# Kernel optimization log

Hardware: AMD Instinct MI355X
Metric: run time of the kernel (lower is better)

Reference implementation:

```python
import jax, jax.numpy as jnp
import numpy as np

B, S, D = 4, 2048, 1024
H, HD = 16, 64
MLP = 4 * D
EPS = 1e-6


def _rms_norm(x, scale):
    var = jnp.mean(jnp.square(x), axis=-1, keepdims=True)
    return x * jax.lax.rsqrt(var + EPS) * scale


def setup_inputs() -> dict:
    key = jax.random.key(0)
    ks = jax.random.split(key, 8)
    sd = D ** -0.5
    return {
        "x": jax.random.normal(ks[0], (B, S, D), jnp.float32),
        "pre_norm_scale": jnp.ones((D,), jnp.float32),
        "w_mlp_in": jax.random.normal(ks[1], (D, MLP), jnp.float32) * sd,   # MLPBlockInput, no bias
        "wq": jax.random.normal(ks[2], (D, H, HD), jnp.float32) * sd,
        "wk": jax.random.normal(ks[3], (D, H, HD), jnp.float32) * sd,
        "wv": jax.random.normal(ks[4], (D, H, HD), jnp.float32) * sd,
        "w_mlp_out": jax.random.normal(ks[5], (MLP, D), jnp.float32) * (MLP ** -0.5),
        "b_mlp_out": jnp.zeros((D,), jnp.float32),
        "w_attn_out": jax.random.normal(ks[6], (H, HD, D), jnp.float32) * sd,  # DenseGeneral axis=(-2,-1)
        "b_attn_out": jnp.zeros((D,), jnp.float32),
    }


def reference(x, pre_norm_scale, w_mlp_in, wq, wk, wv, w_mlp_out, b_mlp_out,
              w_attn_out, b_attn_out):
    residual = x
    xn = _rms_norm(x, pre_norm_scale)                      # pre_norm (TPNorm)

    # QKVMLPDense: fused MLP-input + QKV projections
    h = jax.nn.gelu(jnp.einsum("bsd,df->bsf", xn, w_mlp_in))   # [B,S,MLP]
    q = jnp.einsum("bsd,dhk->bshk", xn, wq)                    # [B,S,H,HD]
    k = jnp.einsum("bsd,dhk->bshk", xn, wk)
    v = jnp.einsum("bsd,dhk->bshk", xn, wv)

    # dot_product_attention (mask=None)
    scores = jnp.einsum("bqhd,bkhd->bhqk", q, k) / jnp.sqrt(jnp.asarray(HD, x.dtype))
    probs = jax.nn.softmax(scores, axis=-1)
    attn_v = jnp.einsum("bhqk,bkhd->bqhd", probs, v)           # [B,S,H,HD]

    # AttnMLPOut: mlp_out + attn_out
    mlp_out = jnp.einsum("bsf,fd->bsd", h, w_mlp_out) + b_mlp_out
    attn_out = jnp.einsum("bqhk,hkd->bqd", attn_v, w_attn_out) + b_attn_out
    block_out = mlp_out + attn_out                              # dropout is identity (train=False)
    return residual + block_out
```

## Files before the change

### kernel.cpp

```cpp
#include <hip/hip_runtime.h>
#include <cstdint>
#include <cstddef>

typedef float floatx4 __attribute__((ext_vector_type(4)));
typedef short bf16x8 __attribute__((ext_vector_type(8)));

#define MFMA(a, b, c) __builtin_amdgcn_mfma_f32_16x16x32_bf16((a), (b), (c), 0, 0, 0)

__device__ __forceinline__ unsigned short f2bf(float f) {
  union { float f; unsigned int u; } v; v.f = f;
  unsigned int u = v.u;
  unsigned int r = (u + 0x7FFFu + ((u >> 16) & 1u)) >> 16;
  return (unsigned short)r;
}

__device__ __forceinline__ void gload_lds16(const unsigned short* g, unsigned short* s) {
  __builtin_amdgcn_global_load_lds(
      (const __attribute__((address_space(1))) unsigned int*)g,
      (__attribute__((address_space(3))) unsigned int*)s, 16, 0, 0);
}

__global__ __launch_bounds__(256) void transpose_cast(
    const float* __restrict__ src, unsigned short* __restrict__ dst,
    int R, int C, int ldd) {
  __shared__ float tile[32][33];
  int bx = blockIdx.x, by = blockIdx.y;
  int tx = threadIdx.x & 31, ty = threadIdx.x >> 5;
#pragma unroll
  for (int i = 0; i < 4; i++) {
    int r = ty + i * 8;
    tile[r][tx] = src[(size_t)(by * 32 + r) * C + bx * 32 + tx];
  }
  __syncthreads();
#pragma unroll
  for (int i = 0; i < 4; i++) {
    int r = ty + i * 8;
    dst[(size_t)(bx * 32 + r) * ldd + by * 32 + tx] = f2bf(tile[tx][r]);
  }
}

__global__ __launch_bounds__(256) void rmsnorm_kernel(
    const float* __restrict__ x, const float* __restrict__ scale,
    unsigned short* __restrict__ xn) {
  int row = blockIdx.x;
  const float4 v = ((const float4*)(x + (size_t)row * 1024))[threadIdx.x];
  float ss = v.x * v.x + v.y * v.y + v.z * v.z + v.w * v.w;
#pragma unroll
  for (int off = 1; off < 64; off <<= 1) ss += __shfl_xor(ss, off, 64);
  __shared__ float ws4[4];
  if ((threadIdx.x & 63) == 0) ws4[threadIdx.x >> 6] = ss;
  __syncthreads();
  float tot = ws4[0] + ws4[1] + ws4[2] + ws4[3];
  float rs = rsqrtf(tot * (1.0f / 1024.0f) + 1e-6f);
  const float4 sc = ((const float4*)scale)[threadIdx.x];
  uint2 o;
  o.x = (unsigned)f2bf(v.x * rs * sc.x) | ((unsigned)f2bf(v.y * rs * sc.y) << 16);
  o.y = (unsigned)f2bf(v.z * rs * sc.z) | ((unsigned)f2bf(v.w * rs * sc.w) << 16);
  ((uint2*)(xn + (size_t)row * 1024))[threadIdx.x] = o;
}

template <int MODE>
__global__ __launch_bounds__(256, 2) void gemm_bt(
    const unsigned short* __restrict__ A, const unsigned short* __restrict__ BT,
    int K, void* __restrict__ outp,
    const float* __restrict__ bias1, const float* __restrict__ bias2,
    const float* __restrict__ resid,
    int msplit, int tm, int tn,
    unsigned short* __restrict__ q_out, unsigned short* __restrict__ k_out,
    unsigned short* __restrict__ v_out) {
  __shared__ unsigned short As[2][128 * 32];
  __shared__ unsigned short Bs[2][128 * 32];

  int id = blockIdx.x + gridDim.x * blockIdx.y;
  int xcd = id & 7, j = id >> 3;
  int mh = xcd % msplit, nq = xcd / msplit;
  int by = mh * tm + j / tn;
  int bx = nq * tn + j % tn;
  int m0 = by * 128, n0 = bx * 128;

  int t = threadIdx.x, lane = t & 63, wave = t >> 6;
  int l15 = lane & 15, quad = lane >> 4;
  int wm = (wave & 1) * 64, wn = (wave >> 1) * 64;

  floatx4 acc[4][4] = {};

  int off0 = wave * 1024 + lane * 8;
  int off1 = off0 + 512;
  int r0 = off0 >> 5, c0 = off0 & 31;
  const unsigned short* gA0 = A + (size_t)(m0 + r0) * K + c0;
  const unsigned short* gA1 = A + (size_t)(m0 + r0 + 16) * K + c0;
  const unsigned short* gB0 = BT + (size_t)(n0 + r0) * K + c0;
  const unsigned short* gB1 = BT + (size_t)(n0 + r0 + 16) * K + c0;
  unsigned short* sA[2] = {&As[0][off0], &As[1][off0]};
  unsigned short* sA_[2] = {&As[0][off1], &As[1][off1]};
  unsigned short* sB[2] = {&Bs[0][off0], &Bs[1][off0]};
  unsigned short* sB_[2] = {&Bs[0][off1], &Bs[1][off1]};

  for (int kt = 0; kt < K; kt += 64) {
    __syncthreads();
#pragma unroll
    for (int kk = 0; kk < 2; kk++) {
      int kg = kt + kk * 32;
      gload_lds16(gA0 + kg, sA[kk]);
      gload_lds16(gA1 + kg, sA_[kk]);
      gload_lds16(gB0 + kg, sB[kk]);
      gload_lds16(gB1 + kg, sB_[kk]);
    }
    __syncthreads();
#pragma unroll
    for (int kk = 0; kk < 2; kk++) {
      bf16x8 a[4], b[4];
#pragma unroll
      for (int im = 0; im < 4; im++)
        a[im] = *(const bf16x8*)&As[kk][(wm + im * 16 + l15) * 32 + quad * 8];
#pragma unroll
      for (int in_ = 0; in_ < 4; in_++)
        b[in_] = *(const bf16x8*)&Bs[kk][(wn + in_ * 16 + l15) * 32 + quad * 8];
#pragma unroll
      for (int im = 0; im < 4; im++)
#pragma unroll
        for (int in_ = 0; in_ < 4; in_++)
          acc[im][in_] = MFMA(a[im], b[in_], acc[im][in_]);
    }
  }

#pragma unroll
  for (int im = 0; im < 4; im++) {
#pragma unroll
    for (int in_ = 0; in_ < 4; in_++) {
#pragma unroll
      for (int r = 0; r < 4; r++) {
        int row = m0 + wm + im * 16 + quad * 4 + r;
        int col = n0 + wn + in_ * 16 + l15;
        float v = acc[im][in_][r];
        if constexpr (MODE == 6) {
          if (n0 < 4096) {
            float z = 0.7978845608028654f * (v + 0.044715f * v * v * v);
            float e = __expf(2.0f * z);
            float th = 1.0f - 2.0f / (e + 1.0f);
            ((unsigned short*)outp)[(size_t)row * 5120 + col] = f2bf(0.5f * v * (1.0f + th));
          } else {
            int seg = (n0 - 4096) >> 10;
            int cs = col - 4096 - (seg << 10);
            int b_ = row >> 11, s = row & 2047, h = cs >> 6, hd = cs & 63;
            if (seg == 0)
              q_out[(((size_t)(b_ * 16 + h)) * 2048 + s) * 64 + hd] = f2bf(v * 0.125f);
            else if (seg == 1)
              k_out[(((size_t)(b_ * 16 + h)) * 2048 + s) * 64 + hd] = f2bf(v);
            else
              v_out[(((size_t)(b_ * 16 + h)) * 64 + hd) * 2048 + s] = f2bf(v);
          }
        } else {
          size_t idx = (size_t)row * 1024 + col;
          ((float*)outp)[idx] = v + bias1[col] + bias2[col] + resid[idx];
        }
      }
    }
  }
}

__global__ __launch_bounds__(256, 2) void flash_attn(
    const unsigned short* __restrict__ q_buf, const unsigned short* __restrict__ k_buf,
    const unsigned short* __restrict__ v_buf, unsigned short* __restrict__ cat) {
  constexpr int S = 2048, HD = 64;
  constexpr int LK = 72, LV = 72, LP = 68;
  __shared__ unsigned short Ks[64 * LK];
  __shared__ unsigned short Vs[64 * LV];
  __shared__ unsigned short Ps[4][32 * LP];

  int id = blockIdx.x + gridDim.x * blockIdx.y;
  int xcd = id & 7, j = id >> 3;
  int bh = xcd * 8 + (j >> 4);
  int qbk = j & 15;

  int t = threadIdx.x, lane = t & 63, wave = t >> 6;
  int l15 = lane & 15, quad = lane >> 4;

  const unsigned short* qp = q_buf + (size_t)bh * S * HD;
  const unsigned short* kp = k_buf + (size_t)bh * S * HD;
  const unsigned short* vp = v_buf + (size_t)bh * HD * S;

  int q0 = qbk * 128 + wave * 32;
  bf16x8 aQ[2][2];
#pragma unroll
  for (int qf = 0; qf < 2; qf++) {
    aQ[qf][0] = *(const bf16x8*)&qp[(size_t)(q0 + qf * 16 + l15) * HD + quad * 8];
    aQ[qf][1] = *(const bf16x8*)&qp[(size_t)(q0 + qf * 16 + l15) * HD + 32 + quad * 8];
  }

  floatx4 acc_o[2][4] = {};
  float lrow[2][4] = {};

  int kr = t >> 3, kc = (t & 7) * 8;

  for (int kv = 0; kv < S; kv += 64) {
    __syncthreads();
#pragma unroll
    for (int i = 0; i < 2; i++) {
      int r = kr + 32 * i;
      *(uint4*)&Ks[r * LK + kc] = *(const uint4*)&kp[(size_t)(kv + r) * HD + kc];
      *(uint4*)&Vs[r * LV + kc] = *(const uint4*)&vp[(size_t)r * S + kv + kc];
    }
    __syncthreads();

    floatx4 z[2][4];
#pragma unroll
    for (int cg = 0; cg < 4; cg++) {
      bf16x8 bk0 = *(const bf16x8*)&Ks[(cg * 16 + l15) * LK + quad * 8];
      bf16x8 bk1 = *(const bf16x8*)&Ks[(cg * 16 + l15) * LK + 32 + quad * 8];
#pragma unroll
      for (int qf = 0; qf < 2; qf++) {
        floatx4 acc = {};
        acc = MFMA(aQ[qf][0], bk0, acc);
        acc = MFMA(aQ[qf][1], bk1, acc);
        z[qf][cg] = acc;
      }
    }
#pragma unroll
    for (int qf = 0; qf < 2; qf++)
#pragma unroll
      for (int cg = 0; cg < 4; cg++)
#pragma unroll
        for (int r = 0; r < 4; r++) {
          float e = __expf(z[qf][cg][r]);
          lrow[qf][r] += e;
          Ps[wave][(qf * 16 + quad * 4 + r) * LP + cg * 16 + l15] = f2bf(e);
        }
    __syncthreads();
#pragma unroll
    for (int c = 0; c < 2; c++) {
      bf16x8 aP[2];
#pragma unroll
      for (int qf = 0; qf < 2; qf++) {
        const unsigned short* pp = &Ps[wave][(qf * 16 + l15) * LP + c * 32 + quad * 8];
        ((uint2*)&aP[qf])[0] = *(const uint2*)pp;
        ((uint2*)&aP[qf])[1] = *(const uint2*)(pp + 4);
      }
#pragma unroll
      for (int n = 0; n < 4; n++) {
        bf16x8 bv = *(const bf16x8*)&Vs[(n * 16 + l15) * LV + c * 32 + quad * 8];
        acc_o[0][n] = MFMA(aP[0], bv, acc_o[0][n]);
        acc_o[1][n] = MFMA(aP[1], bv, acc_o[1][n]);
      }
    }
  }

#pragma unroll
  for (int qf = 0; qf < 2; qf++)
#pragma unroll
    for (int r = 0; r < 4; r++) {
      float s = lrow[qf][r];
#pragma unroll
      for (int off = 1; off < 16; off <<= 1) s += __shfl_xor(s, off, 16);
      lrow[qf][r] = s;
    }

  int b_ = bh >> 4, h = bh & 15;
#pragma unroll
  for (int qf = 0; qf < 2; qf++)
#pragma unroll
    for (int r = 0; r < 4; r++) {
      float inv = 1.0f / lrow[qf][r];
      int srow = q0 + qf * 16 + quad * 4 + r;
      size_t base = ((size_t)(b_ * 2048 + srow)) * 5120 + 4096 + h * 64;
#pragma unroll
      for (int n = 0; n < 4; n++)
        cat[base + n * 16 + l15] = f2bf(acc_o[qf][n][r] * inv);
    }
}

extern "C" void kernel_launch(void* const* d_in, const int* in_sizes, int n_in,
                              void* d_out, int out_size, void* d_ws, size_t ws_size,
                              hipStream_t stream) {
  (void)in_sizes; (void)n_in; (void)out_size; (void)ws_size;
  const float* x          = (const float*)d_in[0];
  const float* pns        = (const float*)d_in[1];
  const float* w_mlp_in   = (const float*)d_in[2];
  const float* wq         = (const float*)d_in[3];
  const float* wk         = (const float*)d_in[4];
  const float* wv         = (const float*)d_in[5];
  const float* w_mlp_out  = (const float*)d_in[6];
  const float* b_mlp_out  = (const float*)d_in[7];
  const float* w_attn_out = (const float*)d_in[8];
  const float* b_attn_out = (const float*)d_in[9];
  float* out = (float*)d_out;

  char* ws = (char*)d_ws;
  size_t off = 0;
  auto alloc = [&](size_t bytes) {
    void* p = ws + off;
    off += (bytes + 255) & ~(size_t)255;
    return p;
  };
  const size_t M = 8192;
  unsigned short* xn     = (unsigned short*)alloc(M * 1024 * 2);
  unsigned short* wcatT  = (unsigned short*)alloc((size_t)7168 * 1024 * 2);
  unsigned short* wcat2T = (unsigned short*)alloc((size_t)1024 * 5120 * 2);
  unsigned short* cat    = (unsigned short*)alloc(M * 5120 * 2);
  unsigned short* qb     = (unsigned short*)alloc(M * 1024 * 2);
  unsigned short* kb     = (unsigned short*)alloc(M * 1024 * 2);
  unsigned short* vb     = (unsigned short*)alloc(M * 1024 * 2);

  transpose_cast<<<dim3(128, 32), 256, 0, stream>>>(w_mlp_in, wcatT, 1024, 4096, 1024);
  transpose_cast<<<dim3(32, 32), 256, 0, stream>>>(wq, wcatT + (size_t)4096 * 1024, 1024, 1024, 1024);
  transpose_cast<<<dim3(32, 32), 256, 0, stream>>>(wk, wcatT + (size_t)5120 * 1024, 1024, 1024, 1024);
  transpose_cast<<<dim3(32, 32), 256, 0, stream>>>(wv, wcatT + (size_t)6144 * 1024, 1024, 1024, 1024);
  transpose_cast<<<dim3(32, 128), 256, 0, stream>>>(w_mlp_out, wcat2T, 4096, 1024, 5120);
  transpose_cast<<<dim3(32, 32), 256, 0, stream>>>(w_attn_out, wcat2T + 4096, 1024, 1024, 5120);

  rmsnorm_kernel<<<dim3(8192), 256, 0, stream>>>(x, pns, xn);

  gemm_bt<6><<<dim3(56, 64), 256, 0, stream>>>(
      xn, wcatT, 1024, cat, nullptr, nullptr, nullptr, 2, 32, 14, qb, kb, vb);

  flash_attn<<<dim3(16, 64), 256, 0, stream>>>(qb, kb, vb, cat);

  gemm_bt<7><<<dim3(8, 64), 256, 0, stream>>>(
      cat, wcat2T, 5120, out, b_mlp_out, b_attn_out, x, 2, 32, 2, nullptr, nullptr, nullptr);
}
```

Before: 553.1 us.

## Double-buffer GEMM K-tiles and register-prefetch attention K/V tiles

The GEMM main loop now steps K by 32 and issues the async global-to-LDS loads for the next K slice into the other buffer before computing on the current one. This cuts the loop from two barriers per 64-K step to one barrier per 32-K step. The attention kernel prefetches the next K/V tile into registers while computing the current tile. It also replaces the block-wide barrier before reading the per-wave P buffer with an LDS wait count. The aim is to hide global memory latency behind MFMA work, in exchange for more registers and a correctness reliance on the barrier draining outstanding async loads.

```diff
diff --git a/kernel.cpp b/kernel.cpp
--- a/kernel.cpp
+++ b/kernel.cpp
@@ -91,37 +91,40 @@
   const unsigned short* gA1 = A + (size_t)(m0 + r0 + 16) * K + c0;
   const unsigned short* gB0 = BT + (size_t)(n0 + r0) * K + c0;
   const unsigned short* gB1 = BT + (size_t)(n0 + r0 + 16) * K + c0;
-  unsigned short* sA[2] = {&As[0][off0], &As[1][off0]};
-  unsigned short* sA_[2] = {&As[0][off1], &As[1][off1]};
-  unsigned short* sB[2] = {&Bs[0][off0], &Bs[1][off0]};
-  unsigned short* sB_[2] = {&Bs[0][off1], &Bs[1][off1]};
-
-  for (int kt = 0; kt < K; kt += 64) {
+  unsigned short* sA0[2] = {&As[0][off0], &As[1][off0]};
+  unsigned short* sA1[2] = {&As[0][off1], &As[1][off1]};
+  unsigned short* sB0[2] = {&Bs[0][off0], &Bs[1][off0]};
+  unsigned short* sB1[2] = {&Bs[0][off1], &Bs[1][off1]};
+
+  gload_lds16(gA0, sA0[0]);
+  gload_lds16(gA1, sA1[0]);
+  gload_lds16(gB0, sB0[0]);
+  gload_lds16(gB1, sB1[0]);
+
+  int nIter = K >> 5;
+  for (int it = 0; it < nIter; it++) {
+    int p = it & 1;
     __syncthreads();
-#pragma unroll
-    for (int kk = 0; kk < 2; kk++) {
-      int kg = kt + kk * 32;
-      gload_lds16(gA0 + kg, sA[kk]);
-      gload_lds16(gA1 + kg, sA_[kk]);
-      gload_lds16(gB0 + kg, sB[kk]);
-      gload_lds16(gB1 + kg, sB_[kk]);
-    }
-    __syncthreads();
-#pragma unroll
-    for (int kk = 0; kk < 2; kk++) {
-      bf16x8 a[4], b[4];
-#pragma unroll
-      for (int im = 0; im < 4; im++)
-        a[im] = *(const bf16x8*)&As[kk][(wm + im * 16 + l15) * 32 + quad * 8];
+    if (it + 1 < nIter) {
+      int kn = (it + 1) << 5;
+      int q = p ^ 1;
+      gload_lds16(gA0 + kn, sA0[q]);
+      gload_lds16(gA1 + kn, sA1[q]);
+      gload_lds16(gB0 + kn, sB0[q]);
+      gload_lds16(gB1 + kn, sB1[q]);
+    }
+    bf16x8 a[4], b[4];
+#pragma unroll
+    for (int im = 0; im < 4; im++)
+      a[im] = *(const bf16x8*)&As[p][(wm + im * 16 + l15) * 32 + quad * 8];
+#pragma unroll
+    for (int in_ = 0; in_ < 4; in_++)
+      b[in_] = *(const bf16x8*)&Bs[p][(wn + in_ * 16 + l15) * 32 + quad * 8];
+#pragma unroll
+    for (int im = 0; im < 4; im++)
 #pragma unroll
       for (int in_ = 0; in_ < 4; in_++)
-        b[in_] = *(const bf16x8*)&Bs[kk][(wn + in_ * 16 + l15) * 32 + quad * 8];
-#pragma unroll
-      for (int im = 0; im < 4; im++)
-#pragma unroll
-        for (int in_ = 0; in_ < 4; in_++)
-          acc[im][in_] = MFMA(a[im], b[in_], acc[im][in_]);
-    }
+        acc[im][in_] = MFMA(a[im], b[in_], acc[im][in_]);
   }
 
 #pragma unroll
@@ -193,15 +196,24 @@
 
   int kr = t >> 3, kc = (t & 7) * 8;
 
+  uint4 rK0 = *(const uint4*)&kp[(size_t)kr * HD + kc];
+  uint4 rK1 = *(const uint4*)&kp[(size_t)(kr + 32) * HD + kc];
+  uint4 rV0 = *(const uint4*)&vp[(size_t)kr * S + kc];
+  uint4 rV1 = *(const uint4*)&vp[(size_t)(kr + 32) * S + kc];
+
   for (int kv = 0; kv < S; kv += 64) {
     __syncthreads();
-#pragma unroll
-    for (int i = 0; i < 2; i++) {
-      int r = kr + 32 * i;
-      *(uint4*)&Ks[r * LK + kc] = *(const uint4*)&kp[(size_t)(kv + r) * HD + kc];
-      *(uint4*)&Vs[r * LV + kc] = *(const uint4*)&vp[(size_t)r * S + kv + kc];
-    }
+    *(uint4*)&Ks[kr * LK + kc] = rK0;
+    *(uint4*)&Ks[(kr + 32) * LK + kc] = rK1;
+    *(uint4*)&Vs[kr * LV + kc] = rV0;
+    *(uint4*)&Vs[(kr + 32) * LV + kc] = rV1;
     __syncthreads();
+    if (kv + 64 < S) {
+      rK0 = *(const uint4*)&kp[(size_t)(kv + 64 + kr) * HD + kc];
+      rK1 = *(const uint4*)&kp[(size_t)(kv + 64 + kr + 32) * HD + kc];
+      rV0 = *(const uint4*)&vp[(size_t)kr * S + kv + 64 + kc];
+      rV1 = *(const uint4*)&vp[(size_t)(kr + 32) * S + kv + 64 + kc];
+    }
 
     floatx4 z[2][4];
 #pragma unroll
@@ -226,7 +238,7 @@
           lrow[qf][r] += e;
           Ps[wave][(qf * 16 + quad * 4 + r) * LP + cg * 16 + l15] = f2bf(e);
         }
-    __syncthreads();
+    asm volatile("s_waitcnt lgkmcnt(0)" ::: "memory");
 #pragma unroll
     for (int c = 0; c < 2; c++) {
       bf16x8 aP[2];
```

New measurement: 566.3 us. 1.02x slower.

## Widen GEMM tiles per wave and prefetch K/V in flash attention

Applied to the files above, without the earlier changes.

The GEMM is templated on tile width and wave count. Each wave now computes a 64x128 sub-tile. The first GEMM uses 128x256 blocks, and the output GEMM uses 128x128 blocks with only two waves. This raises the MFMA-to-LDS-load ratio, at the cost of doubled accumulator registers and fewer, larger blocks. Flash attention now register-prefetches the next K/V tile during compute. It also replaces the barrier before reading P with an lgkmcnt wait, which is valid because each wave reads only its own P slice.

```diff
diff --git a/kernel.cpp b/kernel.cpp
--- a/kernel.cpp
+++ b/kernel.cpp
@@ -59,8 +59,8 @@
   ((uint2*)(xn + (size_t)row * 1024))[threadIdx.x] = o;
 }
 
-template <int MODE>
-__global__ __launch_bounds__(256, 2) void gemm_bt(
+template <int MODE, int BN, int NWAVES>
+__global__ __launch_bounds__(NWAVES * 64, 2) void gemm_bt(
     const unsigned short* __restrict__ A, const unsigned short* __restrict__ BT,
     int K, void* __restrict__ outp,
     const float* __restrict__ bias1, const float* __restrict__ bias2,
@@ -68,58 +68,71 @@
     int msplit, int tm, int tn,
     unsigned short* __restrict__ q_out, unsigned short* __restrict__ k_out,
     unsigned short* __restrict__ v_out) {
+  constexpr int CA = 128 / 16 / NWAVES;
+  constexpr int CB = BN / 16 / NWAVES;
   __shared__ unsigned short As[2][128 * 32];
-  __shared__ unsigned short Bs[2][128 * 32];
+  __shared__ unsigned short Bs[2][BN * 32];
 
   int id = blockIdx.x + gridDim.x * blockIdx.y;
   int xcd = id & 7, j = id >> 3;
   int mh = xcd % msplit, nq = xcd / msplit;
   int by = mh * tm + j / tn;
   int bx = nq * tn + j % tn;
-  int m0 = by * 128, n0 = bx * 128;
+  int m0 = by * 128, n0 = bx * BN;
 
   int t = threadIdx.x, lane = t & 63, wave = t >> 6;
   int l15 = lane & 15, quad = lane >> 4;
-  int wm = (wave & 1) * 64, wn = (wave >> 1) * 64;
-
-  floatx4 acc[4][4] = {};
-
-  int off0 = wave * 1024 + lane * 8;
-  int off1 = off0 + 512;
-  int r0 = off0 >> 5, c0 = off0 & 31;
-  const unsigned short* gA0 = A + (size_t)(m0 + r0) * K + c0;
-  const unsigned short* gA1 = A + (size_t)(m0 + r0 + 16) * K + c0;
-  const unsigned short* gB0 = BT + (size_t)(n0 + r0) * K + c0;
-  const unsigned short* gB1 = BT + (size_t)(n0 + r0 + 16) * K + c0;
-  unsigned short* sA[2] = {&As[0][off0], &As[1][off0]};
-  unsigned short* sA_[2] = {&As[0][off1], &As[1][off1]};
-  unsigned short* sB[2] = {&Bs[0][off0], &Bs[1][off0]};
-  unsigned short* sB_[2] = {&Bs[0][off1], &Bs[1][off1]};
+  int wm = (wave & 1) * 64;
+  int wn = (wave >> 1) * 128;
+
+  floatx4 acc[4][8] = {};
+
+  int la = lane * 8;
+  int lr = la >> 5;
+  int lc = la & 31;
+  const unsigned short* gA[CA];
+  const unsigned short* gB[CB];
+  unsigned short* sAp[2][CA];
+  unsigned short* sBp[2][CB];
+#pragma unroll
+  for (int i = 0; i < CA; i++) {
+    int ch = wave * CA + i;
+    gA[i] = A + (size_t)(m0 + ch * 16 + lr) * K + lc;
+    sAp[0][i] = &As[0][ch * 512 + la];
+    sAp[1][i] = &As[1][ch * 512 + la];
+  }
+#pragma unroll
+  for (int i = 0; i < CB; i++) {
+    int ch = wave * CB + i;
+    gB[i] = BT + (size_t)(n0 + ch * 16 + lr) * K + lc;
+    sBp[0][i] = &Bs[0][ch * 512 + la];
+    sBp[1][i] = &Bs[1][ch * 512 + la];
+  }
 
   for (int kt = 0; kt < K; kt += 64) {
     __syncthreads();
 #pragma unroll
     for (int kk = 0; kk < 2; kk++) {
       int kg = kt + kk * 32;
-      gload_lds16(gA0 + kg, sA[kk]);
-      gload_lds16(gA1 + kg, sA_[kk]);
-      gload_lds16(gB0 + kg, sB[kk]);
-      gload_lds16(gB1 + kg, sB_[kk]);
+#pragma unroll
+      for (int i = 0; i < CA; i++) gload_lds16(gA[i] + kg, sAp[kk][i]);
+#pragma unroll
+      for (int i = 0; i < CB; i++) gload_lds16(gB[i] + kg, sBp[kk][i]);
     }
     __syncthreads();
 #pragma unroll
     for (int kk = 0; kk < 2; kk++) {
-      bf16x8 a[4], b[4];
+      bf16x8 a[4], b[8];
 #pragma unroll
       for (int im = 0; im < 4; im++)
         a[im] = *(const bf16x8*)&As[kk][(wm + im * 16 + l15) * 32 + quad * 8];
 #pragma unroll
-      for (int in_ = 0; in_ < 4; in_++)
+      for (int in_ = 0; in_ < 8; in_++)
         b[in_] = *(const bf16x8*)&Bs[kk][(wn + in_ * 16 + l15) * 32 + quad * 8];
 #pragma unroll
       for (int im = 0; im < 4; im++)
 #pragma unroll
-        for (int in_ = 0; in_ < 4; in_++)
+        for (int in_ = 0; in_ < 8; in_++)
           acc[im][in_] = MFMA(a[im], b[in_], acc[im][in_]);
     }
   }
@@ -127,7 +140,7 @@
 #pragma unroll
   for (int im = 0; im < 4; im++) {
 #pragma unroll
-    for (int in_ = 0; in_ < 4; in_++) {
+    for (int in_ = 0; in_ < 8; in_++) {
 #pragma unroll
       for (int r = 0; r < 4; r++) {
         int row = m0 + wm + im * 16 + quad * 4 + r;
@@ -193,15 +206,24 @@
 
   int kr = t >> 3, kc = (t & 7) * 8;
 
+  uint4 rK0 = *(const uint4*)&kp[(size_t)kr * HD + kc];
+  uint4 rK1 = *(const uint4*)&kp[(size_t)(kr + 32) * HD + kc];
+  uint4 rV0 = *(const uint4*)&vp[(size_t)kr * S + kc];
+  uint4 rV1 = *(const uint4*)&vp[(size_t)(kr + 32) * S + kc];
+
   for (int kv = 0; kv < S; kv += 64) {
     __syncthreads();
-#pragma unroll
-    for (int i = 0; i < 2; i++) {
-      int r = kr + 32 * i;
-      *(uint4*)&Ks[r * LK + kc] = *(const uint4*)&kp[(size_t)(kv + r) * HD + kc];
-      *(uint4*)&Vs[r * LV + kc] = *(const uint4*)&vp[(size_t)r * S + kv + kc];
-    }
+    *(uint4*)&Ks[kr * LK + kc] = rK0;
+    *(uint4*)&Ks[(kr + 32) * LK + kc] = rK1;
+    *(uint4*)&Vs[kr * LV + kc] = rV0;
+    *(uint4*)&Vs[(kr + 32) * LV + kc] = rV1;
     __syncthreads();
+    if (kv + 64 < S) {
+      rK0 = *(const uint4*)&kp[(size_t)(kv + 64 + kr) * HD + kc];
+      rK1 = *(const uint4*)&kp[(size_t)(kv + 64 + kr + 32) * HD + kc];
+      rV0 = *(const uint4*)&vp[(size_t)kr * S + kv + 64 + kc];
+      rV1 = *(const uint4*)&vp[(size_t)(kr + 32) * S + kv + 64 + kc];
+    }
 
     floatx4 z[2][4];
 #pragma unroll
@@ -226,7 +248,7 @@
           lrow[qf][r] += e;
           Ps[wave][(qf * 16 + quad * 4 + r) * LP + cg * 16 + l15] = f2bf(e);
         }
-    __syncthreads();
+    asm volatile("s_waitcnt lgkmcnt(0)" ::: "memory");
 #pragma unroll
     for (int c = 0; c < 2; c++) {
       bf16x8 aP[2];
@@ -310,11 +332,11 @@
 
   rmsnorm_kernel<<<dim3(8192), 256, 0, stream>>>(x, pns, xn);
 
-  gemm_bt<6><<<dim3(56, 64), 256, 0, stream>>>(
-      xn, wcatT, 1024, cat, nullptr, nullptr, nullptr, 2, 32, 14, qb, kb, vb);
+  gemm_bt<6, 256, 4><<<dim3(28, 64), 256, 0, stream>>>(
+      xn, wcatT, 1024, cat, nullptr, nullptr, nullptr, 2, 32, 7, qb, kb, vb);
 
   flash_attn<<<dim3(16, 64), 256, 0, stream>>>(qb, kb, vb, cat);
 
-  gemm_bt<7><<<dim3(8, 64), 256, 0, stream>>>(
+  gemm_bt<7, 128, 2><<<dim3(8, 64), 128, 0, stream>>>(
       cat, wcat2T, 5120, out, b_mlp_out, b_attn_out, x, 2, 32, 2, nullptr, nullptr, nullptr);
 }
```

Result: slower. 567.4 us (+2.6%).
